# Performance work log

Hardware: AMD Instinct MI355X
Metric: run time of the kernel (lower is better)

The kernel has to match this reference:

```python
import jax, jax.numpy as jnp
import numpy as np

B, N, CI, CP, H, W, R = 2, 8192, 64, 64, 128, 128, 4
D = (CI + CP) // R  # qk channels = 32
BN_EPS = 1e-5


def setup_inputs() -> dict:
    key = jax.random.key(0)
    ks = jax.random.split(key, 8)
    pts_img = jax.random.uniform(ks[0], (B, N, 2), minval=-1.0, maxval=1.0)
    img_feats = jax.random.normal(ks[1], (B, CI, H, W), dtype=jnp.float32)
    pts_feats = jax.random.normal(ks[2], (B, CP, N), dtype=jnp.float32)
    qk_w = jax.random.normal(ks[3], (D, CI + CP), dtype=jnp.float32) * 0.05
    v_w = jax.random.normal(ks[4], (CP, CP), dtype=jnp.float32) * 0.05
    v_b = jnp.zeros((CP,), dtype=jnp.float32)
    t_w = jax.random.normal(ks[5], (CP, CP), dtype=jnp.float32) * 0.05
    t_b = jnp.zeros((CP,), dtype=jnp.float32)
    bn_gamma = jnp.ones((CP,), dtype=jnp.float32)
    bn_beta = jnp.zeros((CP,), dtype=jnp.float32)
    return dict(pts_img=pts_img, img_feats=img_feats, pts_feats=pts_feats,
                qk_w=qk_w, v_w=v_w, v_b=v_b, t_w=t_w, t_b=t_b,
                bn_gamma=bn_gamma, bn_beta=bn_beta)


def _grid_sample(img_feats, pts_img):
    # torch.nn.functional.grid_sample: bilinear, zeros padding, align_corners=False
    # img_feats [B,C,H,W], pts_img [B,N,2] with (x,y) in [-1,1] -> [B,C,N]
    ix = (pts_img[..., 0] + 1.0) * 0.5 * W - 0.5
    iy = (pts_img[..., 1] + 1.0) * 0.5 * H - 0.5
    x0 = jnp.floor(ix); y0 = jnp.floor(iy)
    x1 = x0 + 1.0;      y1 = y0 + 1.0
    wx1 = ix - x0; wx0 = 1.0 - wx1
    wy1 = iy - y0; wy0 = 1.0 - wy1

    def gather(imgb, yi, xi):  # imgb [C,H,W]; yi,xi [N] float corner coords
        valid = ((xi >= 0) & (xi <= W - 1) & (yi >= 0) & (yi <= H - 1)).astype(imgb.dtype)
        xc = jnp.clip(xi, 0, W - 1).astype(jnp.int32)
        yc = jnp.clip(yi, 0, H - 1).astype(jnp.int32)
        return imgb[:, yc, xc] * valid  # [C,N], zeros outside

    def per_batch(imgb, x0, x1, y0, y1, wx0, wx1, wy0, wy1):
        return (gather(imgb, y0, x0) * (wy0 * wx0) + gather(imgb, y0, x1) * (wy0 * wx1)
                + gather(imgb, y1, x0) * (wy1 * wx0) + gather(imgb, y1, x1) * (wy1 * wx1))

    return jax.vmap(per_batch)(img_feats, x0, x1, y0, y1, wx0, wx1, wy0, wy1)


def reference(pts_img, img_feats, pts_feats, qk_w, v_w, v_b, t_w, t_b, bn_gamma, bn_beta):
    # grid-sample image features at point projections, concat with point features
    pts_wise_img = _grid_sample(img_feats, pts_img)                 # [B,CI,N]
    fusion = jnp.concatenate([pts_wise_img, pts_feats], axis=1)     # [B,CI+CP,N]

    # shared-weight 1x1 conv Q/K (bias=False), V with bias
    x_q = jnp.einsum('dc,bcn->bnd', qk_w, fusion)                   # [B,N,D]
    x_k = jnp.einsum('dc,bcn->bdn', qk_w, fusion)                   # [B,D,N]
    x_v = jnp.einsum('oc,bcn->bon', v_w, pts_feats) + v_b[None, :, None]  # [B,CP,N]

    energy = jnp.einsum('bnd,bdm->bnm', x_q, x_k)                   # [B,N,N]
    attention = jax.nn.softmax(energy, axis=-1)
    # L1 renormalization over rows (dim=1): divide each column by its column-sum
    attention = attention / (1e-9 + attention.sum(axis=1, keepdims=True))

    x_r = jnp.einsum('bcn,bnm->bcm', x_v, attention)                # [B,CP,N]

    # trans_conv(pts_feats - x_r) -> BatchNorm1d (training stats) -> ReLU
    y = jnp.einsum('oc,bcn->bon', t_w, pts_feats - x_r) + t_b[None, :, None]
    mean = y.mean(axis=(0, 2), keepdims=True)
    var = y.var(axis=(0, 2), keepdims=True)  # biased, matching torch BN
    y = (y - mean) * jax.lax.rsqrt(var + BN_EPS)
    y = y * bn_gamma[None, :, None] + bn_beta[None, :, None]
    x_r_out = jax.nn.relu(y)

    return pts_feats + x_r_out
```

## Files before the change

### kernel.cpp

```cpp
#include <hip/hip_runtime.h>
#include <math.h>

#define BB 2
#define NN 8192
#define CI 64
#define CP 64
#define HH 128
#define WW 128
#define DD 32
#define CF 128
#define SPLITM 8
#define SPLITN 2

typedef __bf16 bf16_t;
typedef __bf16 bf16x8 __attribute__((ext_vector_type(8)));
typedef __bf16 bf16x4 __attribute__((ext_vector_type(4)));
typedef float f32x4 __attribute__((ext_vector_type(4)));

#define SQ_L2E 1.2011224087864498f

__device__ __forceinline__ float fexp2(float x) { return __builtin_amdgcn_exp2f(x); }

__device__ __forceinline__ bf16x8 pack8(float a0,float a1,float a2,float a3,
                                        float b0,float b1,float b2,float b3){
    bf16x8 r;
    r[0]=(bf16_t)a0; r[1]=(bf16_t)a1; r[2]=(bf16_t)a2; r[3]=(bf16_t)a3;
    r[4]=(bf16_t)b0; r[5]=(bf16_t)b1; r[6]=(bf16_t)b2; r[7]=(bf16_t)b3;
    return r;
}

__device__ __forceinline__ bf16x8 ld_av(const bf16_t* p){
    bf16x4 lo = *(const bf16x4*)p;
    bf16x4 hi = *(const bf16x4*)(p + 16);
    bf16x8 r;
    r[0]=lo[0];r[1]=lo[1];r[2]=lo[2];r[3]=lo[3];
    r[4]=hi[0];r[5]=hi[1];r[6]=hi[2];r[7]=hi[3];
    return r;
}

__device__ __forceinline__ void gload_lds16(const void* g, void* l) {
    __builtin_amdgcn_global_load_lds(
        (const __attribute__((address_space(1))) unsigned int*)g,
        (__attribute__((address_space(3))) unsigned int*)l, 16, 0, 0);
}

__global__ __launch_bounds__(256) void k_timg(const float* __restrict__ img, float* __restrict__ imgT) {
    __shared__ float tile[64][65];
    int b = blockIdx.y;
    int pos0 = blockIdx.x * 64;
    int tid = threadIdx.x;
    int q = tid >> 6, r = tid & 63;
    const float* src = img + (size_t)b * CI * (HH * WW);
#pragma unroll
    for (int cc = 0; cc < 16; ++cc) {
        int c = cc * 4 + q;
        tile[c][r] = src[(size_t)c * (HH * WW) + pos0 + r];
    }
    __syncthreads();
    float* dst = imgT + ((size_t)b * (HH * WW) + pos0) * 64;
#pragma unroll
    for (int pp = 0; pp < 16; ++pp) {
        int pos = pp * 4 + q;
        dst[(size_t)pos * 64 + r] = tile[r][pos];
    }
}

__global__ __launch_bounds__(256) void k_fuse(
    const float* __restrict__ pts_img, const float* __restrict__ imgT,
    const float* __restrict__ pfeat, const float* __restrict__ qkw,
    const float* __restrict__ vw, const float* __restrict__ vb,
    bf16_t* __restrict__ Qb, bf16_t* __restrict__ XVb)
{
    __shared__ __align__(16) float qk_l[DD * 132];
    __shared__ __align__(16) float vw_l[CP * 68];
    __shared__ __align__(16) float fus[16][CF];
    __shared__ bf16_t xvout[64][20];
    int tid = threadIdx.x;
    for (int i = tid; i < DD * CF; i += 256) qk_l[(i >> 7) * 132 + (i & 127)] = qkw[i];
    for (int i = tid; i < CP * CP; i += 256) vw_l[(i >> 6) * 68 + (i & 63)] = vw[i];

    int w = tid >> 6, l = tid & 63;
    int p0 = blockIdx.x * 16;
    int bb = p0 / NN, n0 = p0 % NN;

#pragma unroll
    for (int i = 0; i < 4; ++i) {
        int pt = i * 4 + w;
        int n = n0 + pt;
        float x = pts_img[(size_t)(p0 + pt) * 2 + 0];
        float y = pts_img[(size_t)(p0 + pt) * 2 + 1];
        float ix = (x + 1.f) * 0.5f * WW - 0.5f;
        float iy = (y + 1.f) * 0.5f * HH - 0.5f;
        float x0 = floorf(ix), y0 = floorf(iy);
        float wx1 = ix - x0, wx0 = 1.f - wx1;
        float wy1 = iy - y0, wy0 = 1.f - wy1;
        int xi0 = (int)x0, yi0 = (int)y0;
        const float* base = imgT + (size_t)bb * (HH * WW) * 64 + l;
        float iv = 0.f;
#pragma unroll
        for (int cr = 0; cr < 4; ++cr) {
            int xi = xi0 + (cr & 1), yi = yi0 + (cr >> 1);
            float wgt = ((cr & 1) ? wx1 : wx0) * ((cr >> 1) ? wy1 : wy0);
            bool v = (xi >= 0) & (xi <= WW - 1) & (yi >= 0) & (yi <= HH - 1);
            int cx = min(max(xi, 0), WW - 1), cy = min(max(yi, 0), HH - 1);
            float s = base[((size_t)cy * WW + cx) * 64];
            iv += (v ? s : 0.f) * wgt;
        }
        float pv = pfeat[((size_t)bb * CP + l) * NN + n];
        fus[pt][l] = iv;
        fus[pt][64 + l] = pv;
    }
    __syncthreads();
#pragma unroll
    for (int i = 0; i < 4; ++i) {
        int pt = i * 4 + w;
        int n = n0 + pt;
        {
            int qo = l & 31, kh = l >> 5;
            const float4* qr = (const float4*)&qk_l[qo * 132 + kh * 64];
            const float4* fp = (const float4*)&fus[pt][kh * 64];
            float acc = 0.f;
#pragma unroll
            for (int k = 0; k < 16; ++k) {
                float4 a = qr[k], bq = fp[k];
                acc += a.x * bq.x + a.y * bq.y + a.z * bq.z + a.w * bq.w;
            }
            acc += __shfl_xor(acc, 32);
            if (kh == 0) Qb[((size_t)bb * NN + n) * DD + qo] = (bf16_t)(acc * SQ_L2E);
        }
        {
            const float4* vr = (const float4*)&vw_l[l * 68];
            const float4* fp = (const float4*)&fus[pt][64];
            float acc = vb[l];
#pragma unroll
            for (int k = 0; k < 16; ++k) {
                float4 a = vr[k], bv = fp[k];
                acc += a.x * bv.x + a.y * bv.y + a.z * bv.z + a.w * bv.w;
            }
            xvout[l][pt] = (bf16_t)acc;
        }
    }
    __syncthreads();
    {
        int c = tid >> 2, seg = (tid & 3) * 4;
        bf16x4 vv;
        vv[0] = xvout[c][seg + 0];
        vv[1] = xvout[c][seg + 1];
        vv[2] = xvout[c][seg + 2];
        vv[3] = xvout[c][seg + 3];
        *(bf16x4*)&XVb[((size_t)bb * CP + c) * NN + n0 + seg] = vv;
    }
}

__global__ __launch_bounds__(256) void k_rowsum(
    const bf16_t* __restrict__ Qb, float* __restrict__ rowsumG)
{
    int b = blockIdx.z;
    int n0 = blockIdx.x * 64;
    int mchunk = blockIdx.y * (NN / SPLITM);
    int tid = threadIdx.x;
    int wv = tid >> 6, l = tid & 63;
    int g = l >> 4, c16 = l & 15;
    const bf16x8* Qv = (const bf16x8*)(Qb + (size_t)b * NN * DD);
    f32x4 z = {0.f, 0.f, 0.f, 0.f};

    bf16x8 A0 = Qv[(size_t)(n0 +  0 + c16) * 4 + g];
    bf16x8 A1 = Qv[(size_t)(n0 + 16 + c16) * 4 + g];
    bf16x8 A2 = Qv[(size_t)(n0 + 32 + c16) * 4 + g];
    bf16x8 A3 = Qv[(size_t)(n0 + 48 + c16) * 4 + g];

    float rs[4][4];
#pragma unroll
    for (int a = 0; a < 4; ++a)
#pragma unroll
        for (int r = 0; r < 4; ++r) rs[a][r] = 0.f;

    int mbase = mchunk + wv * 64;
    bf16x8 Bn0 = Qv[(size_t)(mbase +  0 + c16) * 4 + g];
    bf16x8 Bn1 = Qv[(size_t)(mbase + 16 + c16) * 4 + g];
    bf16x8 Bn2 = Qv[(size_t)(mbase + 32 + c16) * 4 + g];
    bf16x8 Bn3 = Qv[(size_t)(mbase + 48 + c16) * 4 + g];

    const int NIT = NN / SPLITM / 256;
    for (int it = 0; it < NIT; ++it) {
        bf16x8 B0 = Bn0, B1 = Bn1, B2 = Bn2, B3 = Bn3;
        int mnext = mbase + 256;
        if (it + 1 < NIT) {
            Bn0 = Qv[(size_t)(mnext +  0 + c16) * 4 + g];
            Bn1 = Qv[(size_t)(mnext + 16 + c16) * 4 + g];
            Bn2 = Qv[(size_t)(mnext + 32 + c16) * 4 + g];
            Bn3 = Qv[(size_t)(mnext + 48 + c16) * 4 + g];
        }
#define ROWSTEP(Aa, a)                                                        \
        {                                                                     \
            f32x4 e0 = __builtin_amdgcn_mfma_f32_16x16x32_bf16(Aa, B0, z, 0, 0, 0); \
            f32x4 e1 = __builtin_amdgcn_mfma_f32_16x16x32_bf16(Aa, B1, z, 0, 0, 0); \
            f32x4 e2 = __builtin_amdgcn_mfma_f32_16x16x32_bf16(Aa, B2, z, 0, 0, 0); \
            f32x4 e3 = __builtin_amdgcn_mfma_f32_16x16x32_bf16(Aa, B3, z, 0, 0, 0); \
            _Pragma("unroll")                                                 \
            for (int r = 0; r < 4; ++r)                                       \
                rs[a][r] += (fexp2(e0[r]) + fexp2(e1[r])) + (fexp2(e2[r]) + fexp2(e3[r])); \
        }
        ROWSTEP(A0, 0) ROWSTEP(A1, 1) ROWSTEP(A2, 2) ROWSTEP(A3, 3)
#undef ROWSTEP
        mbase = mnext;
    }
#pragma unroll
    for (int a = 0; a < 4; ++a)
#pragma unroll
        for (int r = 0; r < 4; ++r) {
            float v = rs[a][r];
            v += __shfl_xor(v, 1);
            v += __shfl_xor(v, 2);
            v += __shfl_xor(v, 4);
            v += __shfl_xor(v, 8);
            if (c16 == 0)
                atomicAdd(&rowsumG[(size_t)b * NN + n0 + 16 * a + 4 * g + r], v);
        }
}

__global__ __launch_bounds__(256) void k_scale(
    const float* __restrict__ rowsumG, const bf16_t* __restrict__ XVb,
    bf16_t* __restrict__ XVs, bf16_t* __restrict__ irsb)
{
    int b = blockIdx.y;
    int cq = blockIdx.z;
    int n = (blockIdx.x * 256 + threadIdx.x) * 4;
    float4 rs = *(const float4*)&rowsumG[(size_t)b * NN + n];
    float ir0 = 1.f / rs.x, ir1 = 1.f / rs.y, ir2 = 1.f / rs.z, ir3 = 1.f / rs.w;
    if (cq == 0) {
        bf16x4 iv;
        iv[0] = (bf16_t)ir0; iv[1] = (bf16_t)ir1; iv[2] = (bf16_t)ir2; iv[3] = (bf16_t)ir3;
        *(bf16x4*)&irsb[(size_t)b * NN + n] = iv;
    }
    const bf16_t* src = XVb + ((size_t)b * CP + cq * 16) * NN + n;
    char* dstbase = (char*)(XVs + ((size_t)b * CP + cq * 16) * NN);
    size_t nb = (size_t)n * 2;
    size_t hi = nb & ~(size_t)255;
    size_t lo = nb & 255;
#pragma unroll
    for (int c = 0; c < 16; ++c) {
        bf16x4 v = *(const bf16x4*)&src[(size_t)c * NN];
        bf16x4 o;
        o[0] = (bf16_t)((float)v[0] * ir0);
        o[1] = (bf16_t)((float)v[1] * ir1);
        o[2] = (bf16_t)((float)v[2] * ir2);
        o[3] = (bf16_t)((float)v[3] * ir3);
        size_t sb = hi | (lo ^ ((size_t)(c & 7) << 4));
        *(bf16x4*)(dstbase + (size_t)c * NN * 2 + sb) = o;
    }
}

__device__ __forceinline__ void stage_tile(const char* xvbase, int n0, char* ldsbuf, int wv, int l) {
#pragma unroll
    for (int k = 0; k < 2; ++k) {
        int R0 = k * 32 + wv * 4;
        int row = R0 + (l >> 4);
        const char* g = xvbase + (size_t)row * (NN * 2) + (size_t)n0 * 2 + (size_t)(l & 15) * 16;
        gload_lds16(g, ldsbuf + R0 * 256);
    }
}

__global__ __launch_bounds__(512, 4) void k_attn(
    const bf16_t* __restrict__ Qb, const bf16_t* __restrict__ XVs,
    const bf16_t* __restrict__ irsb,
    bf16_t* __restrict__ part, float* __restrict__ cpart)
{
    __shared__ __align__(16) char lds[4 * 64 * 72 * 2];
    __shared__ float csL[4 * 64];

    int b = blockIdx.z;
    int m0 = blockIdx.x * 64;
    int chunk = blockIdx.y;
    int tid = threadIdx.x;
    int wv = tid >> 6, l = tid & 63;
    int g = l >> 4, c16 = l & 15;
    int q4 = wv & 3;
    int jh = wv >> 2;

    const bf16x8* Qv = (const bf16x8*)(Qb + (size_t)b * NN * DD);
    const char* xvbase = (const char*)(XVs + (size_t)b * CP * NN);
    const bf16_t* irow = irsb + (size_t)b * NN;

    bf16x8 bqA = Qv[(size_t)(m0 + jh * 32 + c16) * 4 + g];
    bf16x8 bqB = Qv[(size_t)(m0 + jh * 32 + 16 + c16) * 4 + g];

    f32x4 z = {0.f, 0.f, 0.f, 0.f};
    f32x4 acc[4][2];
    f32x4 acsA = z, acsB = z;
#pragma unroll
    for (int ci = 0; ci < 4; ++ci) { acc[ci][0] = z; acc[ci][1] = z; }

    const int NT = (NN / SPLITN) / 128;
    int nbase = chunk * (NN / SPLITN);

    stage_tile(xvbase, nbase, lds, wv, l);
    int nw0 = nbase + q4 * 32;
    bf16x8 aN0 = Qv[(size_t)(nw0 + c16) * 4 + g];
    bf16x8 aN1 = Qv[(size_t)(nw0 + 16 + c16) * 4 + g];
    bf16x8 cifC = ld_av(irow + nw0 + 4 * g);

    f32x4 EA0 = __builtin_amdgcn_mfma_f32_16x16x32_bf16(aN0, bqA, z, 0, 0, 0);
    f32x4 EA1 = __builtin_amdgcn_mfma_f32_16x16x32_bf16(aN1, bqA, z, 0, 0, 0);
    f32x4 EB0 = __builtin_amdgcn_mfma_f32_16x16x32_bf16(aN0, bqB, z, 0, 0, 0);
    f32x4 EB1 = __builtin_amdgcn_mfma_f32_16x16x32_bf16(aN1, bqB, z, 0, 0, 0);

    int nw1 = nbase + 128 + q4 * 32;
    aN0 = Qv[(size_t)(nw1 + c16) * 4 + g];
    aN1 = Qv[(size_t)(nw1 + 16 + c16) * 4 + g];
    bf16x8 cifN = ld_av(irow + nw1 + 4 * g);
    __syncthreads();

    const int swz = (c16 & 7) << 4;
    const int blo = (q4 * 32 + 4 * g) * 2;
    const int lo_off = blo ^ swz;
    const int hi_off = (blo + 32) ^ swz;

    for (int t = 0; t < NT; ++t) {
        char* buf = lds + (t & 1) * 16384;
        if (t + 1 < NT)
            stage_tile(xvbase, nbase + (t + 1) * 128, lds + ((t + 1) & 1) * 16384, wv, l);

        bf16x8 bpA = pack8(fexp2(EA0[0]), fexp2(EA0[1]), fexp2(EA0[2]), fexp2(EA0[3]),
                           fexp2(EA1[0]), fexp2(EA1[1]), fexp2(EA1[2]), fexp2(EA1[3]));
        bf16x8 bpB = pack8(fexp2(EB0[0]), fexp2(EB0[1]), fexp2(EB0[2]), fexp2(EB0[3]),
                           fexp2(EB1[0]), fexp2(EB1[1]), fexp2(EB1[2]), fexp2(EB1[3]));

        if (t + 1 < NT) {
            EA0 = __builtin_amdgcn_mfma_f32_16x16x32_bf16(aN0, bqA, z, 0, 0, 0);
            EA1 = __builtin_amdgcn_mfma_f32_16x16x32_bf16(aN1, bqA, z, 0, 0, 0);
            EB0 = __builtin_amdgcn_mfma_f32_16x16x32_bf16(aN0, bqB, z, 0, 0, 0);
            EB1 = __builtin_amdgcn_mfma_f32_16x16x32_bf16(aN1, bqB, z, 0, 0, 0);
        }
        bf16x8 cifU = cifC;
        if (t + 2 < NT) {
            int nw2 = nbase + (t + 2) * 128 + q4 * 32;
            aN0 = Qv[(size_t)(nw2 + c16) * 4 + g];
            aN1 = Qv[(size_t)(nw2 + 16 + c16) * 4 + g];
            cifC = cifN;
            cifN = ld_av(irow + nw2 + 4 * g);
        } else {
            cifC = cifN;
        }

        __builtin_amdgcn_s_setprio(1);
        acsA = __builtin_amdgcn_mfma_f32_16x16x32_bf16(cifU, bpA, acsA, 0, 0, 0);
        acsB = __builtin_amdgcn_mfma_f32_16x16x32_bf16(cifU, bpB, acsB, 0, 0, 0);
#pragma unroll
        for (int ci = 0; ci < 4; ++ci) {
            const char* rp = buf + (16 * ci + c16) * 256;
            bf16x4 lo = *(const bf16x4*)(rp + lo_off);
            bf16x4 hi = *(const bf16x4*)(rp + hi_off);
            bf16x8 xv;
            xv[0]=lo[0];xv[1]=lo[1];xv[2]=lo[2];xv[3]=lo[3];
            xv[4]=hi[0];xv[5]=hi[1];xv[6]=hi[2];xv[7]=hi[3];
            acc[ci][0] = __builtin_amdgcn_mfma_f32_16x16x32_bf16(xv, bpA, acc[ci][0], 0, 0, 0);
            acc[ci][1] = __builtin_amdgcn_mfma_f32_16x16x32_bf16(xv, bpB, acc[ci][1], 0, 0, 0);
        }
        __builtin_amdgcn_s_setprio(0);
        __syncthreads();
    }

    if (l < 16) {
        csL[q4 * 64 + 16 * (2 * jh + 0) + l] = acsA[0];
        csL[q4 * 64 + 16 * (2 * jh + 1) + l] = acsB[0];
    }
    bf16_t* epi = (bf16_t*)lds;
#pragma unroll
    for (int ci = 0; ci < 4; ++ci)
#pragma unroll
        for (int jj = 0; jj < 2; ++jj)
#pragma unroll
            for (int r = 0; r < 4; ++r) {
                int cc = 16 * ci + 4 * g + r;
                int mm = jh * 32 + jj * 16 + c16;
                epi[((size_t)q4 * 64 + cc) * 72 + mm] = (bf16_t)acc[ci][jj][r];
            }
    __syncthreads();
    {
        int c = tid >> 3, m8 = (tid & 7) * 8;
        float s[8] = {0.f,0.f,0.f,0.f,0.f,0.f,0.f,0.f};
#pragma unroll
        for (int q = 0; q < 4; ++q) {
            bf16x8 v = *(const bf16x8*)&epi[((size_t)q * 64 + c) * 72 + m8];
#pragma unroll
            for (int i = 0; i < 8; ++i) s[i] += (float)v[i];
        }
        bf16x8 o;
#pragma unroll
        for (int i = 0; i < 8; ++i) o[i] = (bf16_t)s[i];
        *(bf16x8*)&part[(((size_t)chunk * BB + b) * CP + c) * NN + m0 + m8] = o;
    }
    if (tid < 64) {
        float cp = csL[tid] + csL[64 + tid] + csL[128 + tid] + csL[192 + tid];
        cpart[((size_t)chunk * BB + b) * NN + m0 + tid] = cp;
    }
}

__global__ __launch_bounds__(256) void k_post(
    const bf16_t* __restrict__ part, const float* __restrict__ cpart,
    const float* __restrict__ pfeat, const float* __restrict__ tw,
    const float* __restrict__ tb, float* __restrict__ Y)
{
    __shared__ float Tl[64][66];
    __shared__ float twt[64][68];
    int tid = threadIdx.x;
    int b = blockIdx.y;
    int n0 = blockIdx.x * 64;
    int nl = tid & 63;
    int grp = tid >> 6;

    for (int i = tid; i < 64 * 64; i += 256)
        twt[i & 63][i >> 6] = tw[i];

    float cs = 0.f;
#pragma unroll
    for (int sp = 0; sp < SPLITN; ++sp)
        cs += cpart[((size_t)sp * BB + b) * NN + n0 + nl];
    float ic = 1.f / (1e-9f + cs);
#pragma unroll
    for (int k = 0; k < 16; ++k) {
        int c = k * 4 + grp;
        float xr = 0.f;
#pragma unroll
        for (int sp = 0; sp < SPLITN; ++sp)
            xr += (float)part[(((size_t)sp * BB + b) * CP + c) * NN + n0 + nl];
        Tl[c][nl] = pfeat[((size_t)b * CP + c) * NN + n0 + nl] - xr * ic;
    }
    __syncthreads();

    float y0 = tb[grp * 16 + 0], y1 = tb[grp * 16 + 1], y2 = tb[grp * 16 + 2], y3 = tb[grp * 16 + 3];
    float y4 = tb[grp * 16 + 4], y5 = tb[grp * 16 + 5], y6 = tb[grp * 16 + 6], y7 = tb[grp * 16 + 7];
    float y8 = tb[grp * 16 + 8], y9 = tb[grp * 16 + 9], yA = tb[grp * 16 +10], yB = tb[grp * 16 +11];
    float yC = tb[grp * 16 +12], yD = tb[grp * 16 +13], yE = tb[grp * 16 +14], yF = tb[grp * 16 +15];
#pragma unroll 4
    for (int c = 0; c < 64; ++c) {
        float t = Tl[c][nl];
        const float4* wr = (const float4*)&twt[c][grp * 16];
        float4 w0 = wr[0], w1 = wr[1], w2 = wr[2], w3 = wr[3];
        y0 += w0.x * t; y1 += w0.y * t; y2 += w0.z * t; y3 += w0.w * t;
        y4 += w1.x * t; y5 += w1.y * t; y6 += w1.z * t; y7 += w1.w * t;
        y8 += w2.x * t; y9 += w2.y * t; yA += w2.z * t; yB += w2.w * t;
        yC += w3.x * t; yD += w3.y * t; yE += w3.z * t; yF += w3.w * t;
    }
    float* yb = Y + ((size_t)b * CP + grp * 16) * NN + n0 + nl;
    yb[0 * NN] = y0;  yb[1 * NN] = y1;  yb[2 * NN] = y2;  yb[3 * NN] = y3;
    yb[4 * NN] = y4;  yb[5 * NN] = y5;  yb[6 * NN] = y6;  yb[7 * NN] = y7;
    yb[8 * NN] = y8;  yb[9 * NN] = y9;  yb[10 * NN] = yA; yb[11 * NN] = yB;
    yb[12 * NN] = yC; yb[13 * NN] = yD; yb[14 * NN] = yE; yb[15 * NN] = yF;
}

__global__ __launch_bounds__(256) void k_bnstat(
    const float* __restrict__ Y, float* __restrict__ bnred)
{
    __shared__ float red[8];
    int tid = threadIdx.x;
    int o = blockIdx.y, b = blockIdx.z;
    const float* row = Y + ((size_t)b * CP + o) * NN + blockIdx.x * 2048 + tid * 8;
    float4 a = *(const float4*)row;
    float4 c4 = *(const float4*)(row + 4);
    float sv = ((a.x + a.y) + (a.z + a.w)) + ((c4.x + c4.y) + (c4.z + c4.w));
    float sq = ((a.x*a.x + a.y*a.y) + (a.z*a.z + a.w*a.w))
             + ((c4.x*c4.x + c4.y*c4.y) + (c4.z*c4.z + c4.w*c4.w));
#pragma unroll
    for (int off = 1; off < 64; off <<= 1) {
        sv += __shfl_xor(sv, off);
        sq += __shfl_xor(sq, off);
    }
    int wv = tid >> 6;
    if ((tid & 63) == 0) { red[wv] = sv; red[4 + wv] = sq; }
    __syncthreads();
    if (tid == 0) {
        atomicAdd(&bnred[o], red[0] + red[1] + red[2] + red[3]);
        atomicAdd(&bnred[64 + o], red[4] + red[5] + red[6] + red[7]);
    }
}

__global__ __launch_bounds__(256) void k_final(
    const float* __restrict__ Y, const float* __restrict__ pfeat,
    const float* __restrict__ gamma, const float* __restrict__ beta,
    const float* __restrict__ bnred, float* __restrict__ out)
{
    int idx4 = blockIdx.x * 256 + threadIdx.x;
    int o = ((idx4 * 4) / NN) & (CP - 1);
    const float invcnt = 1.f / (float)(BB * NN);
    float mean = bnred[o] * invcnt;
    float var = bnred[64 + o] * invcnt - mean * mean;
    float sc = gamma[o] * rsqrtf(var + 1e-5f);
    float sh = beta[o] - mean * sc;
    float4 y = ((const float4*)Y)[idx4];
    float4 p = ((const float4*)pfeat)[idx4];
    float4 r;
    r.x = p.x + fmaxf(y.x * sc + sh, 0.f);
    r.y = p.y + fmaxf(y.y * sc + sh, 0.f);
    r.z = p.z + fmaxf(y.z * sc + sh, 0.f);
    r.w = p.w + fmaxf(y.w * sc + sh, 0.f);
    ((float4*)out)[idx4] = r;
}

extern "C" void kernel_launch(void* const* d_in, const int* in_sizes, int n_in,
                              void* d_out, int out_size, void* d_ws, size_t ws_size,
                              hipStream_t stream) {
    const float* pts_img = (const float*)d_in[0];
    const float* img     = (const float*)d_in[1];
    const float* pfeat   = (const float*)d_in[2];
    const float* qkw     = (const float*)d_in[3];
    const float* vw      = (const float*)d_in[4];
    const float* vb      = (const float*)d_in[5];
    const float* tw      = (const float*)d_in[6];
    const float* tb      = (const float*)d_in[7];
    const float* gamma   = (const float*)d_in[8];
    const float* beta    = (const float*)d_in[9];

    char* base = (char*)d_ws;
    bf16_t* Qb      = (bf16_t*)(base);
    bf16_t* XVb     = (bf16_t*)(base + 1048576);
    bf16_t* XVs     = (bf16_t*)(base + 3145728);
    float*  rowsumG = (float*)(base + 5251072);
    float*  bn      = (float*)(base + 5316608);
    bf16_t* irsb    = (bf16_t*)(base + 5317120);
    float*  cpart   = (float*)(base + 5349888);
    float*  Y       = (float*)(base + 5874176);
    bf16_t* part    = (bf16_t*)(base + 10068480);
    float*  imgT    = (float*)(base + 26845696);

    hipMemsetAsync(base + 5251072, 0, 66048, stream);
    k_timg<<<dim3((HH * WW) / 64, BB), 256, 0, stream>>>(img, imgT);
    k_fuse<<<(BB * NN) / 16, 256, 0, stream>>>(pts_img, imgT, pfeat, qkw, vw, vb, Qb, XVb);
    k_rowsum<<<dim3(NN / 64, SPLITM, BB), 256, 0, stream>>>(Qb, rowsumG);
    k_scale<<<dim3(NN / 1024, BB, 4), 256, 0, stream>>>(rowsumG, XVb, XVs, irsb);
    k_attn<<<dim3(NN / 64, SPLITN, BB), 512, 0, stream>>>(Qb, XVs, irsb, part, cpart);
    k_post<<<dim3(NN / 64, BB), 256, 0, stream>>>(part, cpart, pfeat, tw, tb, Y);
    k_bnstat<<<dim3(NN / 2048, CP, BB), 256, 0, stream>>>(Y, bn);
    k_final<<<(BB * CP * NN) / 1024, 256, 0, stream>>>(Y, pfeat, gamma, beta, bn, (float*)d_out);
}
```

Before: 115.6 us.

## Use MFMA for Q/V projections in fuse kernel and relax main loop barrier

The fuse kernel drops its LDS-staged fp32 weight copies and scalar dot products. It stores the fused features as bf16 and computes the Q and V projections with bf16 MFMA, reading the weights directly from global memory. In the attention loop the tail prefetch branch is made unconditional, reloading a harmless in-range address on the last iterations. The full __syncthreads is replaced by a partial vmcnt wait plus s_barrier so later prefetch loads can stay in flight. This trades fp32 precision for bf16 in the projections and relies on a hand-tuned waitcnt count being correct for the LDS staging.

```diff
diff --git a/kernel.cpp b/kernel.cpp
--- a/kernel.cpp
+++ b/kernel.cpp
@@ -71,14 +71,8 @@
     const float* __restrict__ vw, const float* __restrict__ vb,
     bf16_t* __restrict__ Qb, bf16_t* __restrict__ XVb)
 {
-    __shared__ __align__(16) float qk_l[DD * 132];
-    __shared__ __align__(16) float vw_l[CP * 68];
-    __shared__ __align__(16) float fus[16][CF];
-    __shared__ bf16_t xvout[64][20];
+    __shared__ __align__(16) bf16_t fusb[16][136];
     int tid = threadIdx.x;
-    for (int i = tid; i < DD * CF; i += 256) qk_l[(i >> 7) * 132 + (i & 127)] = qkw[i];
-    for (int i = tid; i < CP * CP; i += 256) vw_l[(i >> 6) * 68 + (i & 63)] = vw[i];
-
     int w = tid >> 6, l = tid & 63;
     int p0 = blockIdx.x * 16;
     int bb = p0 / NN, n0 = p0 % NN;
@@ -107,48 +101,52 @@
             iv += (v ? s : 0.f) * wgt;
         }
         float pv = pfeat[((size_t)bb * CP + l) * NN + n];
-        fus[pt][l] = iv;
-        fus[pt][64 + l] = pv;
-    }
-    __syncthreads();
-#pragma unroll
-    for (int i = 0; i < 4; ++i) {
-        int pt = i * 4 + w;
-        int n = n0 + pt;
-        {
-            int qo = l & 31, kh = l >> 5;
-            const float4* qr = (const float4*)&qk_l[qo * 132 + kh * 64];
-            const float4* fp = (const float4*)&fus[pt][kh * 64];
-            float acc = 0.f;
-#pragma unroll
-            for (int k = 0; k < 16; ++k) {
-                float4 a = qr[k], bq = fp[k];
-                acc += a.x * bq.x + a.y * bq.y + a.z * bq.z + a.w * bq.w;
-            }
-            acc += __shfl_xor(acc, 32);
-            if (kh == 0) Qb[((size_t)bb * NN + n) * DD + qo] = (bf16_t)(acc * SQ_L2E);
-        }
-        {
-            const float4* vr = (const float4*)&vw_l[l * 68];
-            const float4* fp = (const float4*)&fus[pt][64];
-            float acc = vb[l];
-#pragma unroll
-            for (int k = 0; k < 16; ++k) {
-                float4 a = vr[k], bv = fp[k];
-                acc += a.x * bv.x + a.y * bv.y + a.z * bv.z + a.w * bv.w;
-            }
-            xvout[l][pt] = (bf16_t)acc;
-        }
-    }
-    __syncthreads();
-    {
-        int c = tid >> 2, seg = (tid & 3) * 4;
-        bf16x4 vv;
-        vv[0] = xvout[c][seg + 0];
-        vv[1] = xvout[c][seg + 1];
-        vv[2] = xvout[c][seg + 2];
-        vv[3] = xvout[c][seg + 3];
-        *(bf16x4*)&XVb[((size_t)bb * CP + c) * NN + n0 + seg] = vv;
+        fusb[pt][l] = (bf16_t)iv;
+        fusb[pt][64 + l] = (bf16_t)pv;
+    }
+    __syncthreads();
+
+    int g = l >> 4, c16 = l & 15;
+    f32x4 z = {0.f, 0.f, 0.f, 0.f};
+    if (w < 2) {
+        const float* wr = qkw + (size_t)(w * 16 + c16) * 128;
+        f32x4 acc = z;
+#pragma unroll
+        for (int kk = 0; kk < 4; ++kk) {
+            float4 a0 = *(const float4*)&wr[kk * 32 + 4 * g];
+            float4 a1 = *(const float4*)&wr[kk * 32 + 16 + 4 * g];
+            bf16x8 af = pack8(a0.x, a0.y, a0.z, a0.w, a1.x, a1.y, a1.z, a1.w);
+            bf16x8 bfr = ld_av(&fusb[c16][kk * 32 + 4 * g]);
+            acc = __builtin_amdgcn_mfma_f32_16x16x32_bf16(af, bfr, acc, 0, 0, 0);
+        }
+        bf16x4 qo;
+#pragma unroll
+        for (int r = 0; r < 4; ++r) qo[r] = (bf16_t)(acc[r] * SQ_L2E);
+        *(bf16x4*)&Qb[((size_t)bb * NN + n0 + c16) * DD + w * 16 + 4 * g] = qo;
+    } else {
+        int vh = w - 2;
+        const float* wrA = vw + (size_t)(vh * 32 + c16) * 64;
+        const float* wrB = vw + (size_t)(vh * 32 + 16 + c16) * 64;
+        f32x4 accA = z, accB = z;
+#pragma unroll
+        for (int kk = 0; kk < 2; ++kk) {
+            bf16x8 bfr = ld_av(&fusb[c16][64 + kk * 32 + 4 * g]);
+            float4 a0 = *(const float4*)&wrA[kk * 32 + 4 * g];
+            float4 a1 = *(const float4*)&wrA[kk * 32 + 16 + 4 * g];
+            accA = __builtin_amdgcn_mfma_f32_16x16x32_bf16(
+                pack8(a0.x, a0.y, a0.z, a0.w, a1.x, a1.y, a1.z, a1.w), bfr, accA, 0, 0, 0);
+            a0 = *(const float4*)&wrB[kk * 32 + 4 * g];
+            a1 = *(const float4*)&wrB[kk * 32 + 16 + 4 * g];
+            accB = __builtin_amdgcn_mfma_f32_16x16x32_bf16(
+                pack8(a0.x, a0.y, a0.z, a0.w, a1.x, a1.y, a1.z, a1.w), bfr, accB, 0, 0, 0);
+        }
+#pragma unroll
+        for (int r = 0; r < 4; ++r) {
+            int oA = vh * 32 + 4 * g + r;
+            int oB = oA + 16;
+            XVb[((size_t)bb * CP + oA) * NN + n0 + c16] = (bf16_t)(accA[r] + vb[oA]);
+            XVb[((size_t)bb * CP + oB) * NN + n0 + c16] = (bf16_t)(accB[r] + vb[oB]);
+        }
     }
 }
 
@@ -333,14 +331,12 @@
             EB1 = __builtin_amdgcn_mfma_f32_16x16x32_bf16(aN1, bqB, z, 0, 0, 0);
         }
         bf16x8 cifU = cifC;
-        if (t + 2 < NT) {
-            int nw2 = nbase + (t + 2) * 128 + q4 * 32;
+        {
+            int nw2 = (t + 2 < NT) ? (nbase + (t + 2) * 128 + q4 * 32) : (nbase + q4 * 32);
             aN0 = Qv[(size_t)(nw2 + c16) * 4 + g];
             aN1 = Qv[(size_t)(nw2 + 16 + c16) * 4 + g];
             cifC = cifN;
             cifN = ld_av(irow + nw2 + 4 * g);
-        } else {
-            cifC = cifN;
         }
 
         __builtin_amdgcn_s_setprio(1);
@@ -358,9 +354,12 @@
             acc[ci][1] = __builtin_amdgcn_mfma_f32_16x16x32_bf16(xv, bpB, acc[ci][1], 0, 0, 0);
         }
         __builtin_amdgcn_s_setprio(0);
-        __syncthreads();
-    }
-
+
+        asm volatile("s_waitcnt vmcnt(4)" ::: "memory");
+        __builtin_amdgcn_s_barrier();
+    }
+
+    __syncthreads();
     if (l < 16) {
         csL[q4 * 64 + 16 * (2 * jh + 0) + l] = acsA[0];
         csL[q4 * 64 + 16 * (2 * jh + 1) + l] = acsB[0];
```

Measured after the change: 105.0 us. 9.2% less time.
